# Optimization experiments

Measured on AMD Instinct MI355X. Metric: run time of the kernel, lower is better.

Reference implementation:

```python
import jax, jax.numpy as jnp
import numpy as np

N = 8192        # batch rows
D = 1024        # final_dim (power of 2, == init_dim so padding = 0)
STACK = 4       # nbr_stack
SIGMA = 1.0


def _hadamard(n):
    H = np.array([[1.0]], dtype=np.float32)
    while H.shape[0] < n:
        H = np.block([[H, H], [H, -H]])
    return H


def setup_inputs() -> dict:
    key = jax.random.key(0)
    x = jax.random.normal(key, (N, D), dtype=jnp.float32)
    rs = np.random.RandomState(0)
    # B: random signs (diag), shape (STACK, D)
    B = jnp.asarray(rs.choice([-1.0, 1.0], size=(STACK, D)).astype(np.float32))
    # G: gaussian diag, flattened to (STACK*D,)
    G2 = rs.randn(STACK, D).astype(np.float32)
    G = jnp.asarray(G2.reshape(STACK * D))
    # S: chi-like scaling normalized by per-stack norm of G, flattened
    G_norm = np.linalg.norm(G2, axis=1, keepdims=True)
    S2 = (np.abs(rs.randn(STACK, D)).astype(np.float32) * np.sqrt(D)) / G_norm
    S = jnp.asarray(S2.reshape(STACK * D).astype(np.float32))
    # H: dense Walsh-Hadamard matrix (D, D), +-1 entries (non-trainable constant)
    H = jnp.asarray(_hadamard(D))
    # P: per-stack permutation with stack offsets, gathered along feature axis
    P = jnp.asarray(np.concatenate([rs.permutation(D) + i * D for i in range(STACK)]).astype(np.int32))
    bias = jnp.zeros((2 * STACK * D,), dtype=jnp.float32)
    return {"x": x, "B": B, "G": G, "S": S, "bias": bias, "H": H, "P": P}


def reference(x, B, G, S, bias, H, P):
    n = x.shape[0]
    # padding = final_dim - init_dim = 0 here; pad kept for faithfulness
    xp = jnp.pad(x.reshape(-1, D), ((0, 0), (0, 0)))
    # diag B then Hadamard matmul: [n, STACK, D]
    h = xp[:, None, :] * B
    h = jnp.einsum('nsd,de->nse', h, H).reshape(n, STACK * D)
    # permutation gather, diag G
    h = h[:, P] * G
    # second Hadamard matmul
    h = jnp.einsum('nsd,de->nse', h.reshape(n, STACK, D), H).reshape(n, STACK * D)
    # scale by 1/(sigma*sqrt(D)) and diag S
    h = (1.0 / (SIGMA * np.sqrt(D))) * h * S
    # cos/sin random-feature activation
    out = np.sqrt(1.0 / D).astype(np.float32) * jnp.concatenate([jnp.cos(h), jnp.sin(h)], axis=1)
    out = out + bias
    return out
```

## Files before the change

### kernel.cpp

```cpp
#include <hip/hip_runtime.h>
#include <math.h>


#define FF_D 1024
#define FF_STACK 4
#define FF_NT 256

__device__ __forceinline__ void bf_pair(float& a, float& b) {
    float s = a + b;
    float d = a - b;
    a = s; b = d;
}

__global__ __launch_bounds__(FF_NT) void fastfood_kernel(
    const float* __restrict__ x,
    const float* __restrict__ Bsign,
    const float* __restrict__ G,
    const float* __restrict__ S,
    const float* __restrict__ bias,
    const int* __restrict__ P,
    float* __restrict__ out)
{
    __shared__ float lds[FF_D];
    const int row  = blockIdx.x;
    const int t    = threadIdx.x;
    const int lane = t & 63;
    const int wave = t >> 6;

    float xr[4];
    #pragma unroll
    for (int k = 0; k < 4; ++k) xr[k] = x[row * FF_D + t + FF_NT * k];

    const float inv_sqrt_d = 0.03125f;

    for (int s = 0; s < FF_STACK; ++s) {
        float v[4];
        #pragma unroll
        for (int k = 0; k < 4; ++k)
            v[k] = xr[k] * Bsign[s * FF_D + t + FF_NT * k];

        #pragma unroll
        for (int st = 1; st <= 32; st <<= 1) {
            #pragma unroll
            for (int k = 0; k < 4; ++k) {
                float p = __shfl_xor(v[k], st, 64);
                v[k] = (lane & st) ? (p - v[k]) : (v[k] + p);
            }
        }
        bf_pair(v[0], v[1]); bf_pair(v[2], v[3]);
        bf_pair(v[0], v[2]); bf_pair(v[1], v[3]);
        __syncthreads();
        #pragma unroll
        for (int k = 0; k < 4; ++k) lds[t + FF_NT * k] = v[k];
        __syncthreads();
        #pragma unroll
        for (int k = 0; k < 4; ++k)
            v[k] = lds[lane + 64 * k + 256 * wave];
        bf_pair(v[0], v[1]); bf_pair(v[2], v[3]);
        bf_pair(v[0], v[2]); bf_pair(v[1], v[3]);
        __syncthreads();
        #pragma unroll
        for (int k = 0; k < 4; ++k) lds[lane + 64 * k + 256 * wave] = v[k];
        __syncthreads();

        #pragma unroll
        for (int k = 0; k < 4; ++k) {
            int j = s * FF_D + t + FF_NT * k;
            v[k] = lds[P[j] & (FF_D - 1)] * G[j];
        }

        #pragma unroll
        for (int st = 1; st <= 32; st <<= 1) {
            #pragma unroll
            for (int k = 0; k < 4; ++k) {
                float p = __shfl_xor(v[k], st, 64);
                v[k] = (lane & st) ? (p - v[k]) : (v[k] + p);
            }
        }
        bf_pair(v[0], v[1]); bf_pair(v[2], v[3]);
        bf_pair(v[0], v[2]); bf_pair(v[1], v[3]);
        __syncthreads();
        #pragma unroll
        for (int k = 0; k < 4; ++k) lds[t + FF_NT * k] = v[k];
        __syncthreads();
        #pragma unroll
        for (int k = 0; k < 4; ++k)
            v[k] = lds[lane + 64 * k + 256 * wave];
        bf_pair(v[0], v[1]); bf_pair(v[2], v[3]);
        bf_pair(v[0], v[2]); bf_pair(v[1], v[3]);

        #pragma unroll
        for (int k = 0; k < 4; ++k) {
            int e = lane + 64 * k + 256 * wave;
            int j = s * FF_D + e;
            float w = v[k] * inv_sqrt_d * S[j];
            float sn, cs;
            __sincosf(w, &sn, &cs);
            long long base = (long long)row * (2 * FF_STACK * FF_D);
            out[base + j] = cs * inv_sqrt_d + bias[j];
            out[base + FF_STACK * FF_D + j] =
                sn * inv_sqrt_d + bias[FF_STACK * FF_D + j];
        }
    }
}

extern "C" void kernel_launch(void* const* d_in, const int* in_sizes, int n_in,
                              void* d_out, int out_size, void* d_ws, size_t ws_size,
                              hipStream_t stream) {
    const float* x    = (const float*)d_in[0];
    const float* B    = (const float*)d_in[1];
    const float* G    = (const float*)d_in[2];
    const float* S    = (const float*)d_in[3];
    const float* bias = (const float*)d_in[4];
    const int*   P    = (const int*)d_in[6];
    float* out = (float*)d_out;

    const int n_rows = in_sizes[0] / FF_D;
    fastfood_kernel<<<n_rows, FF_NT, 0, stream>>>(x, B, G, S, bias, P, out);
}
```

Measured before the change: 343.7 us.

## Assign one wave per row with register-resident FWHT and swizzled LDS transposes

```diff
diff --git a/kernel.cpp b/kernel.cpp
--- a/kernel.cpp
+++ b/kernel.cpp
@@ -5,101 +5,146 @@
 #define FF_D 1024
 #define FF_STACK 4
 #define FF_NT 256
+#define ROWS_PER_BLOCK 4
 
-__device__ __forceinline__ void bf_pair(float& a, float& b) {
-    float s = a + b;
-    float d = a - b;
-    a = s; b = d;
+__device__ __forceinline__ int swz(int e) { return e ^ (((e >> 6) & 7) << 2); }
+
+#define STAGE_BIT(vv, m) { \
+    _Pragma("unroll") \
+    for (int i_ = 0; i_ < 16; ++i_) \
+        if (!(i_ & (m))) { \
+            float s_ = vv[i_] + vv[i_ | (m)]; \
+            float d_ = vv[i_] - vv[i_ | (m)]; \
+            vv[i_] = s_; vv[i_ | (m)] = d_; \
+        } \
 }
 
 __global__ __launch_bounds__(FF_NT) void fastfood_kernel(
     const float* __restrict__ x,
-    const float* __restrict__ Bsign,
+    const float* __restrict__ Bs,
     const float* __restrict__ G,
     const float* __restrict__ S,
     const float* __restrict__ bias,
-    const int* __restrict__ P,
+    const int*   __restrict__ P,
     float* __restrict__ out)
 {
-    __shared__ float lds[FF_D];
-    const int row  = blockIdx.x;
-    const int t    = threadIdx.x;
-    const int lane = t & 63;
-    const int wave = t >> 6;
+    __shared__ float lds[ROWS_PER_BLOCK * FF_D];
+    const int lane = threadIdx.x & 63;
+    const int wave = threadIdx.x >> 6;
+    const int row  = blockIdx.x * ROWS_PER_BLOCK + wave;
+    float* wl = lds + (wave << 10);
 
-    float xr[4];
+    float xr[16];
     #pragma unroll
-    for (int k = 0; k < 4; ++k) xr[k] = x[row * FF_D + t + FF_NT * k];
+    for (int q = 0; q < 4; ++q) {
+        const float4 t = *(const float4*)&x[((long long)row << 10) + (q << 8) + (lane << 2)];
+        xr[4*q+0] = t.x; xr[4*q+1] = t.y; xr[4*q+2] = t.z; xr[4*q+3] = t.w;
+    }
 
-    const float inv_sqrt_d = 0.03125f;
+    const int eB = (lane & 3) | ((lane & 60) << 4);
+    const float kout = 0.03125f;
+    const float karg = 0.03125f * 0.15915494309f;
 
     for (int s = 0; s < FF_STACK; ++s) {
-        float v[4];
-        #pragma unroll
-        for (int k = 0; k < 4; ++k)
-            v[k] = xr[k] * Bsign[s * FF_D + t + FF_NT * k];
+        const int sb = s << 10;
+        float v[16];
 
         #pragma unroll
-        for (int st = 1; st <= 32; st <<= 1) {
-            #pragma unroll
-            for (int k = 0; k < 4; ++k) {
-                float p = __shfl_xor(v[k], st, 64);
-                v[k] = (lane & st) ? (p - v[k]) : (v[k] + p);
-            }
-        }
-        bf_pair(v[0], v[1]); bf_pair(v[2], v[3]);
-        bf_pair(v[0], v[2]); bf_pair(v[1], v[3]);
-        __syncthreads();
-        #pragma unroll
-        for (int k = 0; k < 4; ++k) lds[t + FF_NT * k] = v[k];
-        __syncthreads();
-        #pragma unroll
-        for (int k = 0; k < 4; ++k)
-            v[k] = lds[lane + 64 * k + 256 * wave];
-        bf_pair(v[0], v[1]); bf_pair(v[2], v[3]);
-        bf_pair(v[0], v[2]); bf_pair(v[1], v[3]);
-        __syncthreads();
-        #pragma unroll
-        for (int k = 0; k < 4; ++k) lds[lane + 64 * k + 256 * wave] = v[k];
-        __syncthreads();
-
-        #pragma unroll
-        for (int k = 0; k < 4; ++k) {
-            int j = s * FF_D + t + FF_NT * k;
-            v[k] = lds[P[j] & (FF_D - 1)] * G[j];
+        for (int q = 0; q < 4; ++q) {
+            const float4 b4 = *(const float4*)&Bs[sb + (q << 8) + (lane << 2)];
+            v[4*q+0] = xr[4*q+0] * b4.x; v[4*q+1] = xr[4*q+1] * b4.y;
+            v[4*q+2] = xr[4*q+2] * b4.z; v[4*q+3] = xr[4*q+3] * b4.w;
         }
 
+        STAGE_BIT(v, 1) STAGE_BIT(v, 2) STAGE_BIT(v, 4) STAGE_BIT(v, 8)
         #pragma unroll
-        for (int st = 1; st <= 32; st <<= 1) {
-            #pragma unroll
-            for (int k = 0; k < 4; ++k) {
-                float p = __shfl_xor(v[k], st, 64);
-                v[k] = (lane & st) ? (p - v[k]) : (v[k] + p);
+        for (int q = 0; q < 4; ++q)
+            *(float4*)&wl[swz((q << 8) | (lane << 2))] =
+                make_float4(v[4*q], v[4*q+1], v[4*q+2], v[4*q+3]);
+        __builtin_amdgcn_wave_barrier();
+        #pragma unroll
+        for (int r = 0; r < 16; ++r) v[r] = wl[swz(eB | (r << 2))];
+        STAGE_BIT(v, 1) STAGE_BIT(v, 2) STAGE_BIT(v, 4) STAGE_BIT(v, 8)
+        __builtin_amdgcn_wave_barrier();
+        #pragma unroll
+        for (int r = 0; r < 16; ++r) wl[swz(eB | (r << 2))] = v[r];
+        __builtin_amdgcn_wave_barrier();
+        #pragma unroll
+        for (int q = 0; q < 4; ++q) {
+            const float4 t = *(const float4*)&wl[swz(((lane & 15) << 2) | (q << 6) | ((lane & 48) << 4))];
+            v[4*q+0] = t.x; v[4*q+1] = t.y; v[4*q+2] = t.z; v[4*q+3] = t.w;
+        }
+        STAGE_BIT(v, 4) STAGE_BIT(v, 8)
+
+        __builtin_amdgcn_wave_barrier();
+        #pragma unroll
+        for (int q = 0; q < 4; ++q)
+            *(float4*)&wl[swz(((lane & 15) << 2) | (q << 6) | ((lane & 48) << 4))] =
+                make_float4(v[4*q], v[4*q+1], v[4*q+2], v[4*q+3]);
+        __builtin_amdgcn_wave_barrier();
+        #pragma unroll
+        for (int q = 0; q < 4; ++q) {
+            const int jb = sb + (q << 8) + (lane << 2);
+            const int4   p4 = *(const int4*)&P[jb];
+            const float4 g4 = *(const float4*)&G[jb];
+            v[4*q+0] = wl[swz(p4.x & (FF_D - 1))] * g4.x;
+            v[4*q+1] = wl[swz(p4.y & (FF_D - 1))] * g4.y;
+            v[4*q+2] = wl[swz(p4.z & (FF_D - 1))] * g4.z;
+            v[4*q+3] = wl[swz(p4.w & (FF_D - 1))] * g4.w;
+        }
+
+        STAGE_BIT(v, 1) STAGE_BIT(v, 2) STAGE_BIT(v, 4) STAGE_BIT(v, 8)
+        __builtin_amdgcn_wave_barrier();
+        #pragma unroll
+        for (int q = 0; q < 4; ++q)
+            *(float4*)&wl[swz((q << 8) | (lane << 2))] =
+                make_float4(v[4*q], v[4*q+1], v[4*q+2], v[4*q+3]);
+        __builtin_amdgcn_wave_barrier();
+        #pragma unroll
+        for (int r = 0; r < 16; ++r) v[r] = wl[swz(eB | (r << 2))];
+        STAGE_BIT(v, 1) STAGE_BIT(v, 2) STAGE_BIT(v, 4) STAGE_BIT(v, 8)
+        __builtin_amdgcn_wave_barrier();
+        #pragma unroll
+        for (int r = 0; r < 16; ++r) wl[swz(eB | (r << 2))] = v[r];
+        __builtin_amdgcn_wave_barrier();
+        #pragma unroll
+        for (int q = 0; q < 4; ++q) {
+            const float4 t = *(const float4*)&wl[swz(((lane & 15) << 2) | (q << 6) | ((lane & 48) << 4))];
+            v[4*q+0] = t.x; v[4*q+1] = t.y; v[4*q+2] = t.z; v[4*q+3] = t.w;
+        }
+        STAGE_BIT(v, 4) STAGE_BIT(v, 8)
+
+        const long long obase = ((long long)row << 13);
+        #pragma unroll
+        for (int q = 0; q < 4; ++q) {
+            const int e0 = ((lane & 15) << 2) | (q << 6) | ((lane & 48) << 4);
+            const int j  = sb + e0;
+            const float4 s4  = *(const float4*)&S[j];
+            const float4 bc4 = *(const float4*)&bias[j];
+            const float4 bs4 = *(const float4*)&bias[FF_STACK * FF_D + j];
+            float4 oc, os;
+            {
+                const float tr = __builtin_amdgcn_fractf(v[4*q+0] * (s4.x * karg));
+                oc.x = __builtin_amdgcn_cosf(tr) * kout + bc4.x;
+                os.x = __builtin_amdgcn_sinf(tr) * kout + bs4.x;
             }
-        }
-        bf_pair(v[0], v[1]); bf_pair(v[2], v[3]);
-        bf_pair(v[0], v[2]); bf_pair(v[1], v[3]);
-        __syncthreads();
-        #pragma unroll
-        for (int k = 0; k < 4; ++k) lds[t + FF_NT * k] = v[k];
-        __syncthreads();
-        #pragma unroll
-        for (int k = 0; k < 4; ++k)
-            v[k] = lds[lane + 64 * k + 256 * wave];
-        bf_pair(v[0], v[1]); bf_pair(v[2], v[3]);
-        bf_pair(v[0], v[2]); bf_pair(v[1], v[3]);
-
-        #pragma unroll
-        for (int k = 0; k < 4; ++k) {
-            int e = lane + 64 * k + 256 * wave;
-            int j = s * FF_D + e;
-            float w = v[k] * inv_sqrt_d * S[j];
-            float sn, cs;
-            __sincosf(w, &sn, &cs);
-            long long base = (long long)row * (2 * FF_STACK * FF_D);
-            out[base + j] = cs * inv_sqrt_d + bias[j];
-            out[base + FF_STACK * FF_D + j] =
-                sn * inv_sqrt_d + bias[FF_STACK * FF_D + j];
+            {
+                const float tr = __builtin_amdgcn_fractf(v[4*q+1] * (s4.y * karg));
+                oc.y = __builtin_amdgcn_cosf(tr) * kout + bc4.y;
+                os.y = __builtin_amdgcn_sinf(tr) * kout + bs4.y;
+            }
+            {
+                const float tr = __builtin_amdgcn_fractf(v[4*q+2] * (s4.z * karg));
+                oc.z = __builtin_amdgcn_cosf(tr) * kout + bc4.z;
+                os.z = __builtin_amdgcn_sinf(tr) * kout + bs4.z;
+            }
+            {
+                const float tr = __builtin_amdgcn_fractf(v[4*q+3] * (s4.w * karg));
+                oc.w = __builtin_amdgcn_cosf(tr) * kout + bc4.w;
+                os.w = __builtin_amdgcn_sinf(tr) * kout + bs4.w;
+            }
+            *(float4*)&out[obase + j] = oc;
+            *(float4*)&out[obase + FF_STACK * FF_D + j] = os;
         }
     }
 }
@@ -116,5 +161,6 @@
     float* out = (float*)d_out;
 
     const int n_rows = in_sizes[0] / FF_D;
-    fastfood_kernel<<<n_rows, FF_NT, 0, stream>>>(x, B, G, S, bias, P, out);
+    const int blocks = n_rows / ROWS_PER_BLOCK;
+    fastfood_kernel<<<blocks, FF_NT, 0, stream>>>(x, B, G, S, bias, P, out);
 }
```

New measurement: 326.0 us. 5.1% less time.
